# Kernel tuning notes

Measured on AMD Instinct MI355X. Metric: run time of the kernel, lower is better.

The kernel has to match this reference:

```python
import jax, jax.numpy as jnp
import numpy as np

# SMPL kinematic tree parents (joint 0 is root)
SMPL_PARENTS = [-1, 0, 0, 0, 1, 2, 3, 4, 5, 6, 7, 8, 9, 9, 9, 12, 13, 14, 16, 17, 18, 19, 20, 21]
NUM_JOINTS = 24


def _rodrigues(axisang):
    # axisang: (B, J, 3) -> (B, J, 3, 3), matching th_posemap_axisang's eps handling
    angle = jnp.linalg.norm(axisang + 1e-8, axis=-1, keepdims=True)  # (B,J,1)
    axis = axisang / angle
    a = angle[..., None]                      # (B,J,1,1)
    c, s = jnp.cos(a), jnp.sin(a)
    x, y, z = axis[..., 0], axis[..., 1], axis[..., 2]
    zero = jnp.zeros_like(x)
    # skew-symmetric cross-product matrix K
    K = jnp.stack([
        jnp.stack([zero, -z, y], axis=-1),
        jnp.stack([z, zero, -x], axis=-1),
        jnp.stack([-y, x, zero], axis=-1),
    ], axis=-2)                               # (B,J,3,3)
    outer = axis[..., :, None] * axis[..., None, :]
    eye = jnp.eye(3, dtype=axisang.dtype)
    return c * eye + (1.0 - c) * outer + s * K


def setup_inputs() -> dict:
    key = jax.random.key(0)
    k1, k2, k3 = jax.random.split(key, 3)
    B, N = 16, 100000
    normals = jax.random.normal(k1, (B, 3, N), dtype=jnp.float32)
    pose = jax.random.normal(k2, (B, 72), dtype=jnp.float32)
    skinning_weights = jax.random.uniform(k3, (B, NUM_JOINTS, N), dtype=jnp.float32)
    return {"normals": normals, "pose": pose, "skinning_weights": skinning_weights}


def reference(normals, pose, skinning_weights):
    B = pose.shape[0]
    rots = _rodrigues(pose.reshape(B, NUM_JOINTS, 3))  # (B,24,3,3)
    # sequential kinematic-chain composition over the fixed 24-joint tree
    results = [rots[:, 0]]
    for i in range(1, NUM_JOINTS):
        results.append(jnp.matmul(results[SMPL_PARENTS[i]], rots[:, i]))
    th_results2 = jnp.stack(results, axis=-1)          # (B,3,3,24)
    # skinning: (B,9,24) @ (B,24,N) -> (B,3,3,N)
    n_T = jnp.einsum('bijk,bkn->bijn', th_results2, skinning_weights)
    # rotate normals: sum over local axis j of n_T[b,i,j,n] * normals[b,j,n]
    n_verts = jnp.einsum('bijn,bjn->bin', n_T, normals)  # (B,3,N)
    return n_verts
```

## Files before the change

### kernel.cpp

```cpp
#include <hip/hip_runtime.h>

#define NUM_JOINTS 24

typedef float fvec4 __attribute__((ext_vector_type(4)));

__device__ __constant__ int d_chain[NUM_JOINTS][9] = {
    {0,-1,-1,-1,-1,-1,-1,-1,-1},
    {0,1,-1,-1,-1,-1,-1,-1,-1},
    {0,2,-1,-1,-1,-1,-1,-1,-1},
    {0,3,-1,-1,-1,-1,-1,-1,-1},
    {0,1,4,-1,-1,-1,-1,-1,-1},
    {0,2,5,-1,-1,-1,-1,-1,-1},
    {0,3,6,-1,-1,-1,-1,-1,-1},
    {0,1,4,7,-1,-1,-1,-1,-1},
    {0,2,5,8,-1,-1,-1,-1,-1},
    {0,3,6,9,-1,-1,-1,-1,-1},
    {0,1,4,7,10,-1,-1,-1,-1},
    {0,2,5,8,11,-1,-1,-1,-1},
    {0,3,6,9,12,-1,-1,-1,-1},
    {0,3,6,9,13,-1,-1,-1,-1},
    {0,3,6,9,14,-1,-1,-1,-1},
    {0,3,6,9,12,15,-1,-1,-1},
    {0,3,6,9,13,16,-1,-1,-1},
    {0,3,6,9,14,17,-1,-1,-1},
    {0,3,6,9,13,16,18,-1,-1},
    {0,3,6,9,14,17,19,-1,-1},
    {0,3,6,9,13,16,18,20,-1},
    {0,3,6,9,14,17,19,21,-1},
    {0,3,6,9,13,16,18,20,22},
    {0,3,6,9,14,17,19,21,23},
};

__device__ __forceinline__ fvec4 fma4(fvec4 a, float s, fvec4 c) {
    fvec4 r;
    r.x = fmaf(a.x, s, c.x); r.y = fmaf(a.y, s, c.y);
    r.z = fmaf(a.z, s, c.z); r.w = fmaf(a.w, s, c.w);
    return r;
}

__global__ __launch_bounds__(256) void skin_fused_kernel(
    const float* __restrict__ normals,
    const float* __restrict__ pose,
    const float* __restrict__ weights,
    float* __restrict__ out,
    int N) {
    __shared__ float L[NUM_JOINTS][9];
    __shared__ fvec4 Rl[NUM_JOINTS][3];

    const int b = blockIdx.y;
    const int tid = threadIdx.x;

    if (tid < NUM_JOINTS) {
        float x = pose[b * 72 + tid * 3 + 0];
        float y = pose[b * 72 + tid * 3 + 1];
        float z = pose[b * 72 + tid * 3 + 2];
        float ax = x + 1e-8f, ay = y + 1e-8f, az = z + 1e-8f;
        float angle = sqrtf(ax * ax + ay * ay + az * az);
        float inv = 1.0f / angle;
        float ux = x * inv, uy = y * inv, uz = z * inv;
        float c = cosf(angle), s = sinf(angle), t = 1.0f - c;
        L[tid][0] = c + t * ux * ux;
        L[tid][1] = t * ux * uy - s * uz;
        L[tid][2] = t * ux * uz + s * uy;
        L[tid][3] = t * uy * ux + s * uz;
        L[tid][4] = c + t * uy * uy;
        L[tid][5] = t * uy * uz - s * ux;
        L[tid][6] = t * uz * ux - s * uy;
        L[tid][7] = t * uz * uy + s * ux;
        L[tid][8] = c + t * uz * uz;
    }
    __syncthreads();

    if (tid < NUM_JOINTS) {
        float G[9];
        int j0 = d_chain[tid][0];
        #pragma unroll
        for (int e = 0; e < 9; e++) G[e] = L[j0][e];
        #pragma unroll
        for (int d = 1; d < 9; d++) {
            int j = d_chain[tid][d];
            if (j >= 0) {
                float T[9];
                #pragma unroll
                for (int r = 0; r < 3; r++) {
                    #pragma unroll
                    for (int cc = 0; cc < 3; cc++) {
                        T[r * 3 + cc] = G[r * 3 + 0] * L[j][0 * 3 + cc]
                                      + G[r * 3 + 1] * L[j][1 * 3 + cc]
                                      + G[r * 3 + 2] * L[j][2 * 3 + cc];
                    }
                }
                #pragma unroll
                for (int e = 0; e < 9; e++) G[e] = T[e];
            }
        }
        float* Rf = (float*)Rl;
        #pragma unroll
        for (int e = 0; e < 9; e++) Rf[tid * 12 + e] = G[e];
    }
    __syncthreads();

    const int q8 = blockIdx.x * blockDim.x + tid;
    const int n8 = N >> 3;
    const int nf4 = N >> 2;

    const fvec4* __restrict__ Wb = (const fvec4*)(weights + (size_t)b * NUM_JOINTS * N);
    const fvec4* __restrict__ Nb = (const fvec4*)(normals + (size_t)b * 3 * N);
    fvec4* __restrict__ Ob = (fvec4*)(out + (size_t)b * 3 * N);

    if (q8 < n8) {
        fvec4 m0[9], m1[9];
        #pragma unroll
        for (int e = 0; e < 9; e++) {
            m0[e] = (fvec4)(0.f);
            m1[e] = (fvec4)(0.f);
        }

        #pragma unroll 4
        for (int k = 0; k < NUM_JOINTS; k++) {
            fvec4 w0 = __builtin_nontemporal_load(&Wb[(size_t)k * nf4 + (q8 << 1)]);
            fvec4 w1 = __builtin_nontemporal_load(&Wb[(size_t)k * nf4 + (q8 << 1) + 1]);
            fvec4 r0 = Rl[k][0];
            fvec4 r1 = Rl[k][1];
            fvec4 r2 = Rl[k][2];
            m0[0] = fma4(w0, r0.x, m0[0]); m1[0] = fma4(w1, r0.x, m1[0]);
            m0[1] = fma4(w0, r0.y, m0[1]); m1[1] = fma4(w1, r0.y, m1[1]);
            m0[2] = fma4(w0, r0.z, m0[2]); m1[2] = fma4(w1, r0.z, m1[2]);
            m0[3] = fma4(w0, r0.w, m0[3]); m1[3] = fma4(w1, r0.w, m1[3]);
            m0[4] = fma4(w0, r1.x, m0[4]); m1[4] = fma4(w1, r1.x, m1[4]);
            m0[5] = fma4(w0, r1.y, m0[5]); m1[5] = fma4(w1, r1.y, m1[5]);
            m0[6] = fma4(w0, r1.z, m0[6]); m1[6] = fma4(w1, r1.z, m1[6]);
            m0[7] = fma4(w0, r1.w, m0[7]); m1[7] = fma4(w1, r1.w, m1[7]);
            m0[8] = fma4(w0, r2.x, m0[8]); m1[8] = fma4(w1, r2.x, m1[8]);
        }

        fvec4 nx0 = __builtin_nontemporal_load(&Nb[(size_t)0 * nf4 + (q8 << 1)]);
        fvec4 nx1 = __builtin_nontemporal_load(&Nb[(size_t)0 * nf4 + (q8 << 1) + 1]);
        fvec4 ny0 = __builtin_nontemporal_load(&Nb[(size_t)1 * nf4 + (q8 << 1)]);
        fvec4 ny1 = __builtin_nontemporal_load(&Nb[(size_t)1 * nf4 + (q8 << 1) + 1]);
        fvec4 nz0 = __builtin_nontemporal_load(&Nb[(size_t)2 * nf4 + (q8 << 1)]);
        fvec4 nz1 = __builtin_nontemporal_load(&Nb[(size_t)2 * nf4 + (q8 << 1) + 1]);

        #pragma unroll
        for (int i = 0; i < 3; i++) {
            fvec4 o0, o1;
            o0.x = fmaf(m0[3*i].x, nx0.x, fmaf(m0[3*i+1].x, ny0.x, m0[3*i+2].x * nz0.x));
            o0.y = fmaf(m0[3*i].y, nx0.y, fmaf(m0[3*i+1].y, ny0.y, m0[3*i+2].y * nz0.y));
            o0.z = fmaf(m0[3*i].z, nx0.z, fmaf(m0[3*i+1].z, ny0.z, m0[3*i+2].z * nz0.z));
            o0.w = fmaf(m0[3*i].w, nx0.w, fmaf(m0[3*i+1].w, ny0.w, m0[3*i+2].w * nz0.w));
            o1.x = fmaf(m1[3*i].x, nx1.x, fmaf(m1[3*i+1].x, ny1.x, m1[3*i+2].x * nz1.x));
            o1.y = fmaf(m1[3*i].y, nx1.y, fmaf(m1[3*i+1].y, ny1.y, m1[3*i+2].y * nz1.y));
            o1.z = fmaf(m1[3*i].z, nx1.z, fmaf(m1[3*i+1].z, ny1.z, m1[3*i+2].z * nz1.z));
            o1.w = fmaf(m1[3*i].w, nx1.w, fmaf(m1[3*i+1].w, ny1.w, m1[3*i+2].w * nz1.w));
            __builtin_nontemporal_store(o0, &Ob[(size_t)i * nf4 + (q8 << 1)]);
            __builtin_nontemporal_store(o1, &Ob[(size_t)i * nf4 + (q8 << 1) + 1]);
        }
    } else if (q8 == n8 && (N & 7) != 0) {
        const float* Rf = (const float*)Rl;
        for (int n = n8 * 8; n < N; n++) {
            float m[9];
            #pragma unroll
            for (int e = 0; e < 9; e++) m[e] = 0.f;
            for (int k = 0; k < NUM_JOINTS; k++) {
                float w = weights[(size_t)b * NUM_JOINTS * N + (size_t)k * N + n];
                #pragma unroll
                for (int e = 0; e < 9; e++) m[e] = fmaf(w, Rf[k * 12 + e], m[e]);
            }
            float vx = normals[(size_t)b * 3 * N + 0 * N + n];
            float vy = normals[(size_t)b * 3 * N + 1 * N + n];
            float vz = normals[(size_t)b * 3 * N + 2 * N + n];
            for (int i = 0; i < 3; i++) {
                out[(size_t)b * 3 * N + (size_t)i * N + n] =
                    fmaf(m[3 * i], vx, fmaf(m[3 * i + 1], vy, m[3 * i + 2] * vz));
            }
        }
    }
}

extern "C" void kernel_launch(void* const* d_in, const int* in_sizes, int n_in,
                              void* d_out, int out_size, void* d_ws, size_t ws_size,
                              hipStream_t stream) {
    const float* normals = (const float*)d_in[0];
    const float* pose = (const float*)d_in[1];
    const float* weights = (const float*)d_in[2];
    float* out = (float*)d_out;

    const int B = in_sizes[1] / 72;
    const int N = in_sizes[0] / (3 * B);

    const int n8 = (N + 7) >> 3;
    const int gx = (n8 + 255) / 256;
    skin_fused_kernel<<<dim3(gx, B), dim3(256), 0, stream>>>(normals, pose, weights, out, N);
}
```

Before: 231.3 us.

## Reorder skinning math to rotate normals per joint, one float4 per thread

Loads the normals first and, for each joint, rotates them by that joint's matrix, then accumulates weight times the result into three output accumulators. This replaces the nine-element blended-matrix accumulation. It also cuts per-thread work from 8 to 4 vertices, adds an occupancy hint to the launch bounds, and switches to fast sin/cos intrinsics. The aim is lower register pressure and more waves in flight for this memory-bound kernel, at the cost of more FMAs per weight and slightly lower accuracy in the angle-to-matrix step.

```diff
diff --git a/kernel.cpp b/kernel.cpp
--- a/kernel.cpp
+++ b/kernel.cpp
@@ -31,14 +31,24 @@
     {0,3,6,9,14,17,19,21,23},
 };
 
-__device__ __forceinline__ fvec4 fma4(fvec4 a, float s, fvec4 c) {
+__device__ __forceinline__ fvec4 fma4s(fvec4 a, float s, fvec4 c) {
     fvec4 r;
     r.x = fmaf(a.x, s, c.x); r.y = fmaf(a.y, s, c.y);
     r.z = fmaf(a.z, s, c.z); r.w = fmaf(a.w, s, c.w);
     return r;
 }
+__device__ __forceinline__ fvec4 fma4v(fvec4 a, fvec4 b, fvec4 c) {
+    fvec4 r;
+    r.x = fmaf(a.x, b.x, c.x); r.y = fmaf(a.y, b.y, c.y);
+    r.z = fmaf(a.z, b.z, c.z); r.w = fmaf(a.w, b.w, c.w);
+    return r;
+}
+__device__ __forceinline__ fvec4 mul4s(fvec4 a, float s) {
+    fvec4 r; r.x = a.x * s; r.y = a.y * s; r.z = a.z * s; r.w = a.w * s;
+    return r;
+}
 
-__global__ __launch_bounds__(256) void skin_fused_kernel(
+__global__ __launch_bounds__(256, 8) void skin_fused_kernel(
     const float* __restrict__ normals,
     const float* __restrict__ pose,
     const float* __restrict__ weights,
@@ -58,7 +68,7 @@
         float angle = sqrtf(ax * ax + ay * ay + az * az);
         float inv = 1.0f / angle;
         float ux = x * inv, uy = y * inv, uz = z * inv;
-        float c = cosf(angle), s = sinf(angle), t = 1.0f - c;
+        float c = __cosf(angle), s = __sinf(angle), t = 1.0f - c;
         L[tid][0] = c + t * ux * ux;
         L[tid][1] = t * ux * uy - s * uz;
         L[tid][2] = t * ux * uz + s * uy;
@@ -100,79 +110,54 @@
     }
     __syncthreads();
 
-    const int q8 = blockIdx.x * blockDim.x + tid;
-    const int n8 = N >> 3;
+    const int q = blockIdx.x * blockDim.x + tid;
     const int nf4 = N >> 2;
 
     const fvec4* __restrict__ Wb = (const fvec4*)(weights + (size_t)b * NUM_JOINTS * N);
     const fvec4* __restrict__ Nb = (const fvec4*)(normals + (size_t)b * 3 * N);
     fvec4* __restrict__ Ob = (fvec4*)(out + (size_t)b * 3 * N);
 
-    if (q8 < n8) {
-        fvec4 m0[9], m1[9];
+    if (q < nf4) {
+        fvec4 nx = __builtin_nontemporal_load(&Nb[(size_t)0 * nf4 + q]);
+        fvec4 ny = __builtin_nontemporal_load(&Nb[(size_t)1 * nf4 + q]);
+        fvec4 nz = __builtin_nontemporal_load(&Nb[(size_t)2 * nf4 + q]);
+
+        fvec4 o0 = (fvec4)(0.f), o1 = (fvec4)(0.f), o2 = (fvec4)(0.f);
+
         #pragma unroll
-        for (int e = 0; e < 9; e++) {
-            m0[e] = (fvec4)(0.f);
-            m1[e] = (fvec4)(0.f);
-        }
-
-        #pragma unroll 4
         for (int k = 0; k < NUM_JOINTS; k++) {
-            fvec4 w0 = __builtin_nontemporal_load(&Wb[(size_t)k * nf4 + (q8 << 1)]);
-            fvec4 w1 = __builtin_nontemporal_load(&Wb[(size_t)k * nf4 + (q8 << 1) + 1]);
+            fvec4 w = __builtin_nontemporal_load(&Wb[(size_t)k * nf4 + q]);
             fvec4 r0 = Rl[k][0];
             fvec4 r1 = Rl[k][1];
             fvec4 r2 = Rl[k][2];
-            m0[0] = fma4(w0, r0.x, m0[0]); m1[0] = fma4(w1, r0.x, m1[0]);
-            m0[1] = fma4(w0, r0.y, m0[1]); m1[1] = fma4(w1, r0.y, m1[1]);
-            m0[2] = fma4(w0, r0.z, m0[2]); m1[2] = fma4(w1, r0.z, m1[2]);
-            m0[3] = fma4(w0, r0.w, m0[3]); m1[3] = fma4(w1, r0.w, m1[3]);
-            m0[4] = fma4(w0, r1.x, m0[4]); m1[4] = fma4(w1, r1.x, m1[4]);
-            m0[5] = fma4(w0, r1.y, m0[5]); m1[5] = fma4(w1, r1.y, m1[5]);
-            m0[6] = fma4(w0, r1.z, m0[6]); m1[6] = fma4(w1, r1.z, m1[6]);
-            m0[7] = fma4(w0, r1.w, m0[7]); m1[7] = fma4(w1, r1.w, m1[7]);
-            m0[8] = fma4(w0, r2.x, m0[8]); m1[8] = fma4(w1, r2.x, m1[8]);
+            fvec4 t0 = fma4s(nx, r0.x, fma4s(ny, r0.y, mul4s(nz, r0.z)));
+            fvec4 t1 = fma4s(nx, r0.w, fma4s(ny, r1.x, mul4s(nz, r1.y)));
+            fvec4 t2 = fma4s(nx, r1.z, fma4s(ny, r1.w, mul4s(nz, r2.x)));
+            o0 = fma4v(w, t0, o0);
+            o1 = fma4v(w, t1, o1);
+            o2 = fma4v(w, t2, o2);
         }
 
-        fvec4 nx0 = __builtin_nontemporal_load(&Nb[(size_t)0 * nf4 + (q8 << 1)]);
-        fvec4 nx1 = __builtin_nontemporal_load(&Nb[(size_t)0 * nf4 + (q8 << 1) + 1]);
-        fvec4 ny0 = __builtin_nontemporal_load(&Nb[(size_t)1 * nf4 + (q8 << 1)]);
-        fvec4 ny1 = __builtin_nontemporal_load(&Nb[(size_t)1 * nf4 + (q8 << 1) + 1]);
-        fvec4 nz0 = __builtin_nontemporal_load(&Nb[(size_t)2 * nf4 + (q8 << 1)]);
-        fvec4 nz1 = __builtin_nontemporal_load(&Nb[(size_t)2 * nf4 + (q8 << 1) + 1]);
-
-        #pragma unroll
-        for (int i = 0; i < 3; i++) {
-            fvec4 o0, o1;
-            o0.x = fmaf(m0[3*i].x, nx0.x, fmaf(m0[3*i+1].x, ny0.x, m0[3*i+2].x * nz0.x));
-            o0.y = fmaf(m0[3*i].y, nx0.y, fmaf(m0[3*i+1].y, ny0.y, m0[3*i+2].y * nz0.y));
-            o0.z = fmaf(m0[3*i].z, nx0.z, fmaf(m0[3*i+1].z, ny0.z, m0[3*i+2].z * nz0.z));
-            o0.w = fmaf(m0[3*i].w, nx0.w, fmaf(m0[3*i+1].w, ny0.w, m0[3*i+2].w * nz0.w));
-            o1.x = fmaf(m1[3*i].x, nx1.x, fmaf(m1[3*i+1].x, ny1.x, m1[3*i+2].x * nz1.x));
-            o1.y = fmaf(m1[3*i].y, nx1.y, fmaf(m1[3*i+1].y, ny1.y, m1[3*i+2].y * nz1.y));
-            o1.z = fmaf(m1[3*i].z, nx1.z, fmaf(m1[3*i+1].z, ny1.z, m1[3*i+2].z * nz1.z));
-            o1.w = fmaf(m1[3*i].w, nx1.w, fmaf(m1[3*i+1].w, ny1.w, m1[3*i+2].w * nz1.w));
-            __builtin_nontemporal_store(o0, &Ob[(size_t)i * nf4 + (q8 << 1)]);
-            __builtin_nontemporal_store(o1, &Ob[(size_t)i * nf4 + (q8 << 1) + 1]);
-        }
-    } else if (q8 == n8 && (N & 7) != 0) {
+        __builtin_nontemporal_store(o0, &Ob[(size_t)0 * nf4 + q]);
+        __builtin_nontemporal_store(o1, &Ob[(size_t)1 * nf4 + q]);
+        __builtin_nontemporal_store(o2, &Ob[(size_t)2 * nf4 + q]);
+    } else if (q == nf4 && (N & 3) != 0) {
         const float* Rf = (const float*)Rl;
-        for (int n = n8 * 8; n < N; n++) {
-            float m[9];
-            #pragma unroll
-            for (int e = 0; e < 9; e++) m[e] = 0.f;
-            for (int k = 0; k < NUM_JOINTS; k++) {
-                float w = weights[(size_t)b * NUM_JOINTS * N + (size_t)k * N + n];
-                #pragma unroll
-                for (int e = 0; e < 9; e++) m[e] = fmaf(w, Rf[k * 12 + e], m[e]);
-            }
+        for (int n = nf4 * 4; n < N; n++) {
             float vx = normals[(size_t)b * 3 * N + 0 * N + n];
             float vy = normals[(size_t)b * 3 * N + 1 * N + n];
             float vz = normals[(size_t)b * 3 * N + 2 * N + n];
-            for (int i = 0; i < 3; i++) {
-                out[(size_t)b * 3 * N + (size_t)i * N + n] =
-                    fmaf(m[3 * i], vx, fmaf(m[3 * i + 1], vy, m[3 * i + 2] * vz));
+            float s0 = 0.f, s1 = 0.f, s2 = 0.f;
+            for (int k = 0; k < NUM_JOINTS; k++) {
+                float w = weights[(size_t)b * NUM_JOINTS * N + (size_t)k * N + n];
+                float t0 = Rf[k*12+0] * vx + Rf[k*12+1] * vy + Rf[k*12+2] * vz;
+                float t1 = Rf[k*12+3] * vx + Rf[k*12+4] * vy + Rf[k*12+5] * vz;
+                float t2 = Rf[k*12+6] * vx + Rf[k*12+7] * vy + Rf[k*12+8] * vz;
+                s0 = fmaf(w, t0, s0); s1 = fmaf(w, t1, s1); s2 = fmaf(w, t2, s2);
             }
+            out[(size_t)b * 3 * N + 0 * N + n] = s0;
+            out[(size_t)b * 3 * N + 1 * N + n] = s1;
+            out[(size_t)b * 3 * N + 2 * N + n] = s2;
         }
     }
 }
@@ -188,7 +173,8 @@
     const int B = in_sizes[1] / 72;
     const int N = in_sizes[0] / (3 * B);
 
-    const int n8 = (N + 7) >> 3;
-    const int gx = (n8 + 255) / 256;
+    const int nf4 = N >> 2;
+    const int slots = nf4 + ((N & 3) ? 1 : 0);
+    const int gx = (slots + 255) / 256;
     skin_fused_kernel<<<dim3(gx, B), dim3(256), 0, stream>>>(normals, pose, weights, out, N);
 }
```

Result: slower. 669.3 us (+189.4%).
